# Performance work log

Measured on AMD Instinct MI355X. Metric: run time of the kernel, lower is better.

Reference implementation:

```python
import jax, jax.numpy as jnp
import numpy as np

N, K, F = 262144, 256, 128
LAMB = 1.0
EPS = 1e-16


def setup_inputs() -> dict:
    key = jax.random.key(0)
    kx, = jax.random.split(key, 1)
    x = jax.random.normal(kx, (N, F), dtype=jnp.float32)
    # Faithful SVD-orthonormal init of cluster centers (num_clusters > feature_size branch)
    rng = np.random.RandomState(0)
    m_np = rng.rand(K, F)
    m_np = m_np.T                      # (F, K) since K > F
    _, _, vh = np.linalg.svd(m_np, full_matrices=False)  # vh: (F, K)
    m_np = vh[:K].T                    # (K, F), orthonormal columns
    m = jnp.asarray(m_np, dtype=jnp.float32)
    s1 = jnp.ones((K,), dtype=jnp.float32)
    s2 = jnp.ones((K,), dtype=jnp.float32)
    return {"x": x, "m": m, "s1": s1, "s2": s2}


def _p_all(x, m, s):
    # x: (N,F), m: (K,F), s: (K,) -> p: (N,K)
    # squared distances via gram expansion (single GEMM instead of per-sample loop)
    d2 = (jnp.sum(x * x, axis=1, keepdims=True)
          + jnp.sum(m * m, axis=1)[None, :]
          - 2.0 * (x @ m.T))
    d2 = jnp.maximum(d2, 0.0)
    logits = -d2 / (s * s)[None, :]
    return jax.nn.softmax(logits, axis=-1)


def _entropy(p):
    # shannon entropy with the original's clamping of p into (0,1)
    p = jnp.clip(p, EPS, 1.0 - EPS)
    return -jnp.sum(p * jnp.log(p), axis=-1)


def reference(x, m, s1, s2):
    # F.normalize(x): L2-normalize rows with eps=1e-12
    xn = x / jnp.maximum(jnp.linalg.norm(x, axis=1, keepdims=True), 1e-12)
    p = _p_all(xn, m, s1)              # (N,K)
    intra = jnp.mean(_entropy(p))      # scalar
    # inter: entropy of the assignment of the mean center against all centers
    xm = jnp.mean(m, axis=0)           # (F,)
    d = jnp.linalg.norm(xm[None, :] - m, axis=1)  # (K,)
    pi = jax.nn.softmax(-((d / s2) ** 2))
    inter = _entropy(pi)
    total = intra - LAMB * inter
    return (total, intra, inter)
```

## Files before the change

### kernel.cpp

```cpp
#include <hip/hip_runtime.h>
#include <hip/hip_bf16.h>


#define N_ROWS 262144

typedef __attribute__((ext_vector_type(8))) short bf16x8;
typedef __attribute__((ext_vector_type(4))) float f32x4;
typedef __attribute__((ext_vector_type(4))) unsigned short u16x4;

__device__ __forceinline__ unsigned short bf16_rne(float x) {
    unsigned int u = __float_as_uint(x);
    u += 0x7FFFu + ((u >> 16) & 1u);
    return (unsigned short)(u >> 16);
}

__device__ __forceinline__ void cvt8(float4 a, float4 b, bf16x8& hi, bf16x8& lo,
                                     float& n2) {
    float xs[8] = {a.x, a.y, a.z, a.w, b.x, b.y, b.z, b.w};
    unsigned hp[4], lp[4];
    #pragma unroll
    for (int p = 0; p < 4; ++p) {
        float e = xs[2*p], o = xs[2*p+1];
        n2 = __builtin_fmaf(e, e, n2);
        n2 = __builtin_fmaf(o, o, n2);
        __hip_bfloat162 hv = __float22bfloat162_rn(make_float2(e, o));
        unsigned hu = *reinterpret_cast<unsigned*>(&hv);
        float ef = __uint_as_float(hu << 16);
        float of = __uint_as_float(hu & 0xffff0000u);
        __hip_bfloat162 lv = __float22bfloat162_rn(make_float2(e - ef, o - of));
        hp[p] = hu;
        lp[p] = *reinterpret_cast<unsigned*>(&lv);
    }
    hi = *reinterpret_cast<bf16x8*>(hp);
    lo = *reinterpret_cast<bf16x8*>(lp);
}

__global__ __launch_bounds__(256) void prep(
    const float* __restrict__ m, const float* __restrict__ s1,
    unsigned short* __restrict__ mhi_g, float* __restrict__ p2_g)
{
    const int t    = threadIdx.x;
    const int lane = t & 63;
    const int k    = blockIdx.x * 8 + (t >> 5);
    const int f4   = t & 31;
    float4 v = reinterpret_cast<const float4*>(m)[k * 32 + f4];
    float pn = v.x*v.x + v.y*v.y + v.z*v.z + v.w*v.w;
    #pragma unroll
    for (int msk = 1; msk <= 16; msk <<= 1) pn += __shfl_xor(pn, msk);
    float sv  = s1[k];
    float isv = 1.0f / (sv * sv);
    if ((lane & 31) == 0) p2_g[k] = (1.0f + pn) * isv;
    const int f0 = f4 << 2;
    const int c = k >> 4, n = k & 15, s = f0 >> 5, blk = (f0 >> 3) & 3, i0 = f0 & 7;
    const int elem = ((c * 4 + s) * 64 + blk * 16 + n) * 8 + i0;
    float xs[4] = {v.x * isv, v.y * isv, v.z * isv, v.w * isv};
    u16x4 hh;
    #pragma unroll
    for (int q = 0; q < 4; ++q) hh[q] = bf16_rne(xs[q]);
    *(u16x4*)(mhi_g + elem) = hh;
}

__global__ __launch_bounds__(256, 3) void fused_main(
    const float* __restrict__ x, const unsigned short* __restrict__ mhi_g,
    const float* __restrict__ p2_g, float* __restrict__ blocksum)
{
    __shared__ float p2s[256];
    __shared__ float part[8][16][4][2];
    __shared__ float entred[4];

    const int tid  = threadIdx.x;
    const int lane = tid & 63;
    const int w    = tid >> 6;
    const int rw   = lane & 15;
    const int blkl = lane >> 4;

    p2s[tid] = p2_g[tid];

    bf16x8 MB[16];
    #pragma unroll
    for (int tt = 0; tt < 4; ++tt)
        #pragma unroll
        for (int s = 0; s < 4; ++s)
            MB[tt*4+s] = *(const bf16x8*)(mhi_g + (((4*w + tt)*4 + s)*64 + lane)*8);

    __syncthreads();

    const float* xb = x + (size_t)(blockIdx.x * 128 + rw) * 128 + blkl * 8;

    float4 PA[3], PB[3];
    #pragma unroll
    for (int g = 0; g < 3; ++g) {
        PA[g] = *(const float4*)(xb + g * 32);
        PB[g] = *(const float4*)(xb + g * 32 + 4);
    }

    f32x4 acc[4];
    float n2 = 0.0f;

    #pragma unroll
    for (int g = 0; g < 32; ++g) {
        const int s = g & 3;
        const int slot = g % 3;
        if (s == 0) {
            #pragma unroll
            for (int tt = 0; tt < 4; ++tt) acc[tt] = f32x4{0.f, 0.f, 0.f, 0.f};
            n2 = 0.0f;
        }
        bf16x8 ah, al;
        cvt8(PA[slot], PB[slot], ah, al, n2);
        if (g + 3 < 32) {
            const int g2 = g + 3;
            const float* p = xb + (size_t)(g2 >> 2) * 2048 + (g2 & 3) * 32;
            PA[slot] = *(const float4*)(p);
            PB[slot] = *(const float4*)(p + 4);
        }
        #pragma unroll
        for (int tt = 0; tt < 4; ++tt) {
            acc[tt] = __builtin_amdgcn_mfma_f32_16x16x32_bf16(MB[tt*4+s], al, acc[tt], 0, 0, 0);
            acc[tt] = __builtin_amdgcn_mfma_f32_16x16x32_bf16(MB[tt*4+s], ah, acc[tt], 0, 0, 0);
        }
        if (s == 3) {
            const int t = g >> 2;
            float nn = n2;
            nn += __shfl_xor(nn, 16);
            nn += __shfl_xor(nn, 32);
            float ar = 2.0f / fmaxf(sqrtf(nn), 1e-12f);
            float S = 0.f, T = 0.f;
            #pragma unroll
            for (int tt = 0; tt < 4; ++tt) {
                f32x4 p2v = *(const f32x4*)&p2s[(4*w + tt)*16 + blkl*4];
                #pragma unroll
                for (int r = 0; r < 4; ++r) {
                    float l = fminf(__builtin_fmaf(ar, acc[tt][r], -p2v[r]), 0.0f);
                    float e = __expf(l);
                    S += e;
                    T = __builtin_fmaf(l, e, T);
                }
            }
            S += __shfl_xor(S, 16);  T += __shfl_xor(T, 16);
            S += __shfl_xor(S, 32);  T += __shfl_xor(T, 32);
            if (blkl == 0)
                *(float2*)&part[t][rw][w][0] = make_float2(S, T);
        }
    }

    __syncthreads();

    float entl = 0.0f;
    if (tid < 128) {
        const int c = tid >> 4, r16 = tid & 15;
        float S = part[c][r16][0][0] + part[c][r16][1][0]
                + part[c][r16][2][0] + part[c][r16][3][0];
        float T = part[c][r16][0][1] + part[c][r16][1][1]
                + part[c][r16][2][1] + part[c][r16][3][1];
        entl = __logf(S) - T / S;
    }
    #pragma unroll
    for (int msk = 1; msk <= 32; msk <<= 1) entl += __shfl_xor(entl, msk);
    if (lane == 0) entred[w] = entl;
    __syncthreads();
    if (tid == 0)
        blocksum[blockIdx.x] = entred[0] + entred[1] + entred[2] + entred[3];
}

__global__ __launch_bounds__(1024) void finalize(
    const float* __restrict__ blocksum, const float* __restrict__ m,
    const float* __restrict__ s2, float* __restrict__ out)
{
    __shared__ float xmp[8][128];
    __shared__ float xm[128];
    __shared__ double dred[16];
    __shared__ float redS[16], redT[16];
    const int tid  = threadIdx.x;
    const int lane = tid & 63;
    const int w    = tid >> 6;

    double ds = (double)blocksum[tid] + (double)blocksum[tid + 1024];
    #pragma unroll
    for (int msk = 1; msk <= 32; msk <<= 1) ds += __shfl_xor(ds, msk);
    if (lane == 0) dred[w] = ds;

    {
        const int f = tid & 127, g = tid >> 7;
        const float* mp = m + (size_t)g * 32 * 128 + f;
        float cs = 0.f;
        #pragma unroll 8
        for (int k = 0; k < 32; ++k) cs += mp[(size_t)k * 128];
        xmp[g][f] = cs;
    }
    __syncthreads();
    if (tid < 128) {
        float s = 0.f;
        #pragma unroll
        for (int g = 0; g < 8; ++g) s += xmp[g][tid];
        xm[tid] = s * (1.0f / 256.0f);
    }
    __syncthreads();

    const int k = tid >> 2, q = tid & 3;
    float d2 = 0.f;
    {
        const float4* mr  = (const float4*)(m + (size_t)k * 128) + q * 8;
        const float4* xv4 = (const float4*)xm + q * 8;
        #pragma unroll
        for (int j = 0; j < 8; ++j) {
            float4 mv = mr[j], xv = xv4[j];
            float dx = xv.x - mv.x, dy = xv.y - mv.y,
                  dz = xv.z - mv.z, dw = xv.w - mv.w;
            d2 += dx*dx + dy*dy + dz*dz + dw*dw;
        }
    }
    d2 += __shfl_xor(d2, 1);
    d2 += __shfl_xor(d2, 2);
    float sv = s2[k];
    float rr = sqrtf(d2) / sv;
    float lg = -(rr * rr);
    float e  = (q == 0) ? __expf(lg) : 0.f;
    float S = e, T = (q == 0) ? lg * e : 0.f;
    #pragma unroll
    for (int msk = 1; msk <= 32; msk <<= 1) {
        S += __shfl_xor(S, msk);
        T += __shfl_xor(T, msk);
    }
    if (lane == 0) { redS[w] = S; redT[w] = T; }
    __syncthreads();
    if (tid == 0) {
        float Sa = 0.f, Ta = 0.f;
        double intra_d = 0.0;
        #pragma unroll
        for (int i = 0; i < 16; ++i) {
            Sa += redS[i]; Ta += redT[i]; intra_d += dred[i];
        }
        float inter = __logf(Sa) - Ta / Sa;
        float intra = (float)(intra_d / (double)N_ROWS);
        out[0] = intra - inter;
        out[1] = intra;
        out[2] = inter;
    }
}

extern "C" void kernel_launch(void* const* d_in, const int* in_sizes, int n_in,
                              void* d_out, int out_size, void* d_ws, size_t ws_size,
                              hipStream_t stream) {
    const float* x  = (const float*)d_in[0];
    const float* m  = (const float*)d_in[1];
    const float* s1 = (const float*)d_in[2];
    const float* s2 = (const float*)d_in[3];
    float* out = (float*)d_out;

    char* ws = (char*)d_ws;
    unsigned short* mhi_g = (unsigned short*)ws;
    float* p2_g     = (float*)(ws + 65536);
    float* blocksum = (float*)(ws + 65536 + 1024);

    prep<<<dim3(32), dim3(256), 0, stream>>>(m, s1, mhi_g, p2_g);
    fused_main<<<dim3(2048), dim3(256), 0, stream>>>(x, mhi_g, p2_g, blocksum);
    finalize<<<dim3(1), dim3(1024), 0, stream>>>(blocksum, m, s2, out);
}
```

Measured before the change: 231.7 us.

## Drop bf16 low-part correction and split centers across eight waves per block

```diff
diff --git a/kernel.cpp b/kernel.cpp
--- a/kernel.cpp
+++ b/kernel.cpp
@@ -14,25 +14,18 @@
     return (unsigned short)(u >> 16);
 }
 
-__device__ __forceinline__ void cvt8(float4 a, float4 b, bf16x8& hi, bf16x8& lo,
-                                     float& n2) {
+__device__ __forceinline__ void cvt8h(float4 a, float4 b, bf16x8& hi, float& n2) {
     float xs[8] = {a.x, a.y, a.z, a.w, b.x, b.y, b.z, b.w};
-    unsigned hp[4], lp[4];
+    unsigned hp[4];
     #pragma unroll
     for (int p = 0; p < 4; ++p) {
         float e = xs[2*p], o = xs[2*p+1];
         n2 = __builtin_fmaf(e, e, n2);
         n2 = __builtin_fmaf(o, o, n2);
         __hip_bfloat162 hv = __float22bfloat162_rn(make_float2(e, o));
-        unsigned hu = *reinterpret_cast<unsigned*>(&hv);
-        float ef = __uint_as_float(hu << 16);
-        float of = __uint_as_float(hu & 0xffff0000u);
-        __hip_bfloat162 lv = __float22bfloat162_rn(make_float2(e - ef, o - of));
-        hp[p] = hu;
-        lp[p] = *reinterpret_cast<unsigned*>(&lv);
+        hp[p] = *reinterpret_cast<unsigned*>(&hv);
     }
     hi = *reinterpret_cast<bf16x8*>(hp);
-    lo = *reinterpret_cast<bf16x8*>(lp);
 }
 
 __global__ __launch_bounds__(256) void prep(
@@ -60,13 +53,13 @@
     *(u16x4*)(mhi_g + elem) = hh;
 }
 
-__global__ __launch_bounds__(256, 3) void fused_main(
+__global__ __launch_bounds__(512, 4) void fused_main(
     const float* __restrict__ x, const unsigned short* __restrict__ mhi_g,
     const float* __restrict__ p2_g, float* __restrict__ blocksum)
 {
     __shared__ float p2s[256];
-    __shared__ float part[8][16][4][2];
-    __shared__ float entred[4];
+    __shared__ float part[8][16][8][2];
+    __shared__ float entred[8];
 
     const int tid  = threadIdx.x;
     const int lane = tid & 63;
@@ -74,14 +67,14 @@
     const int rw   = lane & 15;
     const int blkl = lane >> 4;
 
-    p2s[tid] = p2_g[tid];
-
-    bf16x8 MB[16];
-    #pragma unroll
-    for (int tt = 0; tt < 4; ++tt)
+    if (tid < 256) p2s[tid] = p2_g[tid];
+
+    bf16x8 MB[8];
+    #pragma unroll
+    for (int tt = 0; tt < 2; ++tt)
         #pragma unroll
         for (int s = 0; s < 4; ++s)
-            MB[tt*4+s] = *(const bf16x8*)(mhi_g + (((4*w + tt)*4 + s)*64 + lane)*8);
+            MB[tt*4+s] = *(const bf16x8*)(mhi_g + (((2*w + tt)*4 + s)*64 + lane)*8);
 
     __syncthreads();
 
@@ -94,7 +87,7 @@
         PB[g] = *(const float4*)(xb + g * 32 + 4);
     }
 
-    f32x4 acc[4];
+    f32x4 acc[2];
     float n2 = 0.0f;
 
     #pragma unroll
@@ -102,33 +95,30 @@
         const int s = g & 3;
         const int slot = g % 3;
         if (s == 0) {
-            #pragma unroll
-            for (int tt = 0; tt < 4; ++tt) acc[tt] = f32x4{0.f, 0.f, 0.f, 0.f};
+            acc[0] = f32x4{0.f, 0.f, 0.f, 0.f};
+            acc[1] = f32x4{0.f, 0.f, 0.f, 0.f};
             n2 = 0.0f;
         }
-        bf16x8 ah, al;
-        cvt8(PA[slot], PB[slot], ah, al, n2);
+        bf16x8 ah;
+        cvt8h(PA[slot], PB[slot], ah, n2);
         if (g + 3 < 32) {
             const int g2 = g + 3;
             const float* p = xb + (size_t)(g2 >> 2) * 2048 + (g2 & 3) * 32;
             PA[slot] = *(const float4*)(p);
             PB[slot] = *(const float4*)(p + 4);
         }
-        #pragma unroll
-        for (int tt = 0; tt < 4; ++tt) {
-            acc[tt] = __builtin_amdgcn_mfma_f32_16x16x32_bf16(MB[tt*4+s], al, acc[tt], 0, 0, 0);
-            acc[tt] = __builtin_amdgcn_mfma_f32_16x16x32_bf16(MB[tt*4+s], ah, acc[tt], 0, 0, 0);
-        }
+        acc[0] = __builtin_amdgcn_mfma_f32_16x16x32_bf16(MB[s],     ah, acc[0], 0, 0, 0);
+        acc[1] = __builtin_amdgcn_mfma_f32_16x16x32_bf16(MB[4 + s], ah, acc[1], 0, 0, 0);
         if (s == 3) {
             const int t = g >> 2;
             float nn = n2;
             nn += __shfl_xor(nn, 16);
             nn += __shfl_xor(nn, 32);
-            float ar = 2.0f / fmaxf(sqrtf(nn), 1e-12f);
+            float ar = 2.0f * __frsqrt_rn(fmaxf(nn, 1e-24f));
             float S = 0.f, T = 0.f;
             #pragma unroll
-            for (int tt = 0; tt < 4; ++tt) {
-                f32x4 p2v = *(const f32x4*)&p2s[(4*w + tt)*16 + blkl*4];
+            for (int tt = 0; tt < 2; ++tt) {
+                f32x4 p2v = *(const f32x4*)&p2s[(2*w + tt)*16 + blkl*4];
                 #pragma unroll
                 for (int r = 0; r < 4; ++r) {
                     float l = fminf(__builtin_fmaf(ar, acc[tt][r], -p2v[r]), 0.0f);
@@ -149,18 +139,24 @@
     float entl = 0.0f;
     if (tid < 128) {
         const int c = tid >> 4, r16 = tid & 15;
-        float S = part[c][r16][0][0] + part[c][r16][1][0]
-                + part[c][r16][2][0] + part[c][r16][3][0];
-        float T = part[c][r16][0][1] + part[c][r16][1][1]
-                + part[c][r16][2][1] + part[c][r16][3][1];
+        float S = 0.f, T = 0.f;
+        #pragma unroll
+        for (int ww = 0; ww < 8; ++ww) {
+            S += part[c][r16][ww][0];
+            T += part[c][r16][ww][1];
+        }
         entl = __logf(S) - T / S;
     }
     #pragma unroll
     for (int msk = 1; msk <= 32; msk <<= 1) entl += __shfl_xor(entl, msk);
     if (lane == 0) entred[w] = entl;
     __syncthreads();
-    if (tid == 0)
-        blocksum[blockIdx.x] = entred[0] + entred[1] + entred[2] + entred[3];
+    if (tid == 0) {
+        float b = 0.f;
+        #pragma unroll
+        for (int i = 0; i < 8; ++i) b += entred[i];
+        blocksum[blockIdx.x] = b;
+    }
 }
 
 __global__ __launch_bounds__(1024) void finalize(
@@ -254,6 +250,6 @@
     float* blocksum = (float*)(ws + 65536 + 1024);
 
     prep<<<dim3(32), dim3(256), 0, stream>>>(m, s1, mhi_g, p2_g);
-    fused_main<<<dim3(2048), dim3(256), 0, stream>>>(x, mhi_g, p2_g, blocksum);
+    fused_main<<<dim3(2048), dim3(512), 0, stream>>>(x, mhi_g, p2_g, blocksum);
     finalize<<<dim3(1), dim3(1024), 0, stream>>>(blocksum, m, s2, out);
 }
```

New measurement: 277.9 us. 20.0% more time.

## Share x bf16 conversion across waves via LDS double buffer, drop lo term

Applied to the files above, without the earlier changes.

```diff
diff --git a/kernel.cpp b/kernel.cpp
--- a/kernel.cpp
+++ b/kernel.cpp
@@ -12,27 +12,6 @@
     unsigned int u = __float_as_uint(x);
     u += 0x7FFFu + ((u >> 16) & 1u);
     return (unsigned short)(u >> 16);
-}
-
-__device__ __forceinline__ void cvt8(float4 a, float4 b, bf16x8& hi, bf16x8& lo,
-                                     float& n2) {
-    float xs[8] = {a.x, a.y, a.z, a.w, b.x, b.y, b.z, b.w};
-    unsigned hp[4], lp[4];
-    #pragma unroll
-    for (int p = 0; p < 4; ++p) {
-        float e = xs[2*p], o = xs[2*p+1];
-        n2 = __builtin_fmaf(e, e, n2);
-        n2 = __builtin_fmaf(o, o, n2);
-        __hip_bfloat162 hv = __float22bfloat162_rn(make_float2(e, o));
-        unsigned hu = *reinterpret_cast<unsigned*>(&hv);
-        float ef = __uint_as_float(hu << 16);
-        float of = __uint_as_float(hu & 0xffff0000u);
-        __hip_bfloat162 lv = __float22bfloat162_rn(make_float2(e - ef, o - of));
-        hp[p] = hu;
-        lp[p] = *reinterpret_cast<unsigned*>(&lv);
-    }
-    hi = *reinterpret_cast<bf16x8*>(hp);
-    lo = *reinterpret_cast<bf16x8*>(lp);
 }
 
 __global__ __launch_bounds__(256) void prep(
@@ -64,6 +43,8 @@
     const float* __restrict__ x, const unsigned short* __restrict__ mhi_g,
     const float* __restrict__ p2_g, float* __restrict__ blocksum)
 {
+    __shared__ unsigned short xfrag[2][2048];
+    __shared__ float n2s[2][16];
     __shared__ float p2s[256];
     __shared__ float part[8][16][4][2];
     __shared__ float entred[4];
@@ -74,6 +55,11 @@
     const int rw   = lane & 15;
     const int blkl = lane >> 4;
 
+    const int sr  = tid >> 4;
+    const int sc  = tid & 15;
+    const int gw0 = (sc >> 2) * 64 + (sc & 3) * 16 + sr;
+    const int gw  = gw0 ^ ((gw0 >> 4) & 7);
+
     p2s[tid] = p2_g[tid];
 
     bf16x8 MB[16];
@@ -83,76 +69,100 @@
         for (int s = 0; s < 4; ++s)
             MB[tt*4+s] = *(const bf16x8*)(mhi_g + (((4*w + tt)*4 + s)*64 + lane)*8);
 
-    __syncthreads();
-
-    const float* xb = x + (size_t)(blockIdx.x * 128 + rw) * 128 + blkl * 8;
-
-    float4 PA[3], PB[3];
-    #pragma unroll
-    for (int g = 0; g < 3; ++g) {
-        PA[g] = *(const float4*)(xb + g * 32);
-        PB[g] = *(const float4*)(xb + g * 32 + 4);
-    }
-
-    f32x4 acc[4];
-    float n2 = 0.0f;
-
-    #pragma unroll
-    for (int g = 0; g < 32; ++g) {
-        const int s = g & 3;
-        const int slot = g % 3;
-        if (s == 0) {
-            #pragma unroll
-            for (int tt = 0; tt < 4; ++tt) acc[tt] = f32x4{0.f, 0.f, 0.f, 0.f};
-            n2 = 0.0f;
-        }
-        bf16x8 ah, al;
-        cvt8(PA[slot], PB[slot], ah, al, n2);
-        if (g + 3 < 32) {
-            const int g2 = g + 3;
-            const float* p = xb + (size_t)(g2 >> 2) * 2048 + (g2 & 3) * 32;
-            PA[slot] = *(const float4*)(p);
-            PB[slot] = *(const float4*)(p + 4);
-        }
+    const float* xrow = x + (size_t)(blockIdx.x * 128 + sr) * 128 + sc * 8;
+
+    {
+        float4 La = *(const float4*)xrow;
+        float4 Lb = *(const float4*)(xrow + 4);
+        float xs[8] = {La.x, La.y, La.z, La.w, Lb.x, Lb.y, Lb.z, Lb.w};
+        float n2p = 0.f;
+        unsigned hp[4];
+        #pragma unroll
+        for (int p = 0; p < 4; ++p) {
+            float e = xs[2*p], o = xs[2*p+1];
+            n2p = __builtin_fmaf(e, e, n2p);
+            n2p = __builtin_fmaf(o, o, n2p);
+            __hip_bfloat162 hv = __float22bfloat162_rn(make_float2(e, o));
+            hp[p] = *reinterpret_cast<unsigned*>(&hv);
+        }
+        *(bf16x8*)&xfrag[0][gw * 8] = *reinterpret_cast<bf16x8*>(hp);
+        #pragma unroll
+        for (int msk = 1; msk <= 8; msk <<= 1) n2p += __shfl_xor(n2p, msk);
+        if (sc == 0) n2s[0][sr] = n2p;
+    }
+    __syncthreads();
+
+    for (int t = 0; t < 8; ++t) {
+        const int cur = t & 1;
+
+        float4 Na, Nb;
+        if (t < 7) {
+            const float* p = xrow + (size_t)(t + 1) * 2048;
+            Na = *(const float4*)p;
+            Nb = *(const float4*)(p + 4);
+        }
+
+        f32x4 acc[4];
+        #pragma unroll
+        for (int tt = 0; tt < 4; ++tt) acc[tt] = f32x4{0.f, 0.f, 0.f, 0.f};
+        #pragma unroll
+        for (int s = 0; s < 4; ++s) {
+            int gr = s * 64 + lane;
+            gr ^= (gr >> 4) & 7;
+            bf16x8 xf = *(const bf16x8*)&xfrag[cur][gr * 8];
+            #pragma unroll
+            for (int tt = 0; tt < 4; ++tt)
+                acc[tt] = __builtin_amdgcn_mfma_f32_16x16x32_bf16(MB[tt*4+s], xf, acc[tt], 0, 0, 0);
+        }
+
+        float nn = n2s[cur][rw];
+        float ar = 2.0f * __frsqrt_rn(fmaxf(nn, 1e-24f));
+        float S = 0.f, T = 0.f;
         #pragma unroll
         for (int tt = 0; tt < 4; ++tt) {
-            acc[tt] = __builtin_amdgcn_mfma_f32_16x16x32_bf16(MB[tt*4+s], al, acc[tt], 0, 0, 0);
-            acc[tt] = __builtin_amdgcn_mfma_f32_16x16x32_bf16(MB[tt*4+s], ah, acc[tt], 0, 0, 0);
-        }
-        if (s == 3) {
-            const int t = g >> 2;
-            float nn = n2;
-            nn += __shfl_xor(nn, 16);
-            nn += __shfl_xor(nn, 32);
-            float ar = 2.0f / fmaxf(sqrtf(nn), 1e-12f);
-            float S = 0.f, T = 0.f;
-            #pragma unroll
-            for (int tt = 0; tt < 4; ++tt) {
-                f32x4 p2v = *(const f32x4*)&p2s[(4*w + tt)*16 + blkl*4];
-                #pragma unroll
-                for (int r = 0; r < 4; ++r) {
-                    float l = fminf(__builtin_fmaf(ar, acc[tt][r], -p2v[r]), 0.0f);
-                    float e = __expf(l);
-                    S += e;
-                    T = __builtin_fmaf(l, e, T);
-                }
+            f32x4 p2v = *(const f32x4*)&p2s[(4*w + tt)*16 + blkl*4];
+            #pragma unroll
+            for (int r = 0; r < 4; ++r) {
+                float l = fminf(__builtin_fmaf(ar, acc[tt][r], -p2v[r]), 0.0f);
+                float e = __expf(l);
+                S += e;
+                T = __builtin_fmaf(l, e, T);
             }
-            S += __shfl_xor(S, 16);  T += __shfl_xor(T, 16);
-            S += __shfl_xor(S, 32);  T += __shfl_xor(T, 32);
-            if (blkl == 0)
-                *(float2*)&part[t][rw][w][0] = make_float2(S, T);
-        }
-    }
-
-    __syncthreads();
+        }
+        S += __shfl_xor(S, 16);  T += __shfl_xor(T, 16);
+        S += __shfl_xor(S, 32);  T += __shfl_xor(T, 32);
+        if (blkl == 0)
+            *(float2*)&part[t][rw][w][0] = make_float2(S, T);
+
+        if (t < 7) {
+            float xs[8] = {Na.x, Na.y, Na.z, Na.w, Nb.x, Nb.y, Nb.z, Nb.w};
+            float n2p = 0.f;
+            unsigned hp[4];
+            #pragma unroll
+            for (int p = 0; p < 4; ++p) {
+                float e = xs[2*p], o = xs[2*p+1];
+                n2p = __builtin_fmaf(e, e, n2p);
+                n2p = __builtin_fmaf(o, o, n2p);
+                __hip_bfloat162 hv = __float22bfloat162_rn(make_float2(e, o));
+                hp[p] = *reinterpret_cast<unsigned*>(&hv);
+            }
+            *(bf16x8*)&xfrag[cur ^ 1][gw * 8] = *reinterpret_cast<bf16x8*>(hp);
+            #pragma unroll
+            for (int msk = 1; msk <= 8; msk <<= 1) n2p += __shfl_xor(n2p, msk);
+            if (sc == 0) n2s[cur ^ 1][sr] = n2p;
+        }
+        __syncthreads();
+    }
 
     float entl = 0.0f;
     if (tid < 128) {
         const int c = tid >> 4, r16 = tid & 15;
-        float S = part[c][r16][0][0] + part[c][r16][1][0]
-                + part[c][r16][2][0] + part[c][r16][3][0];
-        float T = part[c][r16][0][1] + part[c][r16][1][1]
-                + part[c][r16][2][1] + part[c][r16][3][1];
+        float S = 0.f, T = 0.f;
+        #pragma unroll
+        for (int ww = 0; ww < 4; ++ww) {
+            S += part[c][r16][ww][0];
+            T += part[c][r16][ww][1];
+        }
         entl = __logf(S) - T / S;
     }
     #pragma unroll
```

New measurement: 204.6 us. -11.7%, faster.
